# Optimization experiments

Hardware: AMD Instinct MI355X
Metric: run time of the kernel (lower is better)

Reference implementation:

```python
import jax, jax.numpy as jnp
import numpy as np

B, L, D_MODEL = 2, 1024, 512
N_LAYERS = 4
D_INNER = 2 * D_MODEL          # expand=2
D_STATE = 16
D_CONV = 4
DT_RANK = D_MODEL // 16        # ceil(512/16)=32
EPS = 1e-5


def layernorm(x, w, b):
    m = jnp.mean(x, axis=-1, keepdims=True)
    v = jnp.var(x, axis=-1, keepdims=True)
    return (x - m) * jax.lax.rsqrt(v + EPS) * w + b


def selective_scan(u, delta, A, Bm, Cm, Dp):
    # u, delta: [b,l,d]; Bm, Cm: [b,l,n]; A: [d,n]; Dp: [d]
    def step(h, inp):
        dt_t, b_t, c_t, u_t = inp            # [b,d],[b,n],[b,n],[b,d]
        dA = jnp.exp(dt_t[:, :, None] * A)   # [b,d,n]
        h = dA * h + (dt_t * u_t)[:, :, None] * b_t[:, None, :]
        y = jnp.einsum('bdn,bn->bd', h, c_t)
        return h, y

    b, l, d = u.shape
    n = A.shape[1]
    h0 = jnp.zeros((b, d, n), u.dtype)
    xs = (jnp.swapaxes(delta, 0, 1), jnp.swapaxes(Bm, 0, 1),
          jnp.swapaxes(Cm, 0, 1), jnp.swapaxes(u, 0, 1))
    _, ys = jax.lax.scan(step, h0, xs)       # ys: [l,b,d]
    return jnp.swapaxes(ys, 0, 1) + u * Dp


def mamba(x, in_w, conv_w, conv_b, xp_w, dtp_w, dtp_b, A_log, Dp, out_w):
    # x: [b,l,D_MODEL]
    xz = x @ in_w.T                          # [b,l,2*d_inner]
    xc, z = jnp.split(xz, 2, axis=-1)
    xc = jnp.swapaxes(xc, 1, 2)              # [b,d_inner,l]
    xc = jax.lax.conv_general_dilated(
        xc, conv_w[:, None, :], (1,), [(D_CONV - 1, 0)],
        feature_group_count=D_INNER,
        dimension_numbers=('NCH', 'OIH', 'NCH')) + conv_b[None, :, None]
    xc = jax.nn.silu(jnp.swapaxes(xc, 1, 2))  # [b,l,d_inner]
    x_dbl = xc @ xp_w.T                       # [b,l,dt_rank+2n]
    dt = x_dbl[..., :DT_RANK]
    Bm = x_dbl[..., DT_RANK:DT_RANK + D_STATE]
    Cm = x_dbl[..., DT_RANK + D_STATE:]
    dt = jax.nn.softplus(dt @ dtp_w.T + dtp_b)
    A = -jnp.exp(A_log)
    y = selective_scan(xc, dt, A, Bm, Cm, Dp)
    y = y * jax.nn.silu(z)
    return y @ out_w.T


def forward(x, in_proj_w, conv_w, conv_b, x_proj_w, dt_proj_w, dt_proj_b,
            A_log, D_param, out_proj_w, ln_w, ln_b, fnorm_w, fnorm_b):
    residual = None
    for i in range(in_proj_w.shape[0]):
        residual = x if residual is None else x + residual
        xn = layernorm(x, ln_w[i], ln_b[i])  # norm of incoming x (as in torch src)
        h1 = mamba(xn, in_proj_w[i, 0], conv_w[i, 0], conv_b[i, 0],
                   x_proj_w[i, 0], dt_proj_w[i, 0], dt_proj_b[i, 0],
                   A_log[i, 0], D_param[i, 0], out_proj_w[i, 0])
        h2 = mamba(jnp.flip(xn, axis=1), in_proj_w[i, 1], conv_w[i, 1],
                   conv_b[i, 1], x_proj_w[i, 1], dt_proj_w[i, 1],
                   dt_proj_b[i, 1], A_log[i, 1], D_param[i, 1],
                   out_proj_w[i, 1])
        x = h1 + h2                           # bi_add: NOT flipped back, faithful
    x = x + residual
    return layernorm(x, fnorm_w, fnorm_b)


def setup_inputs() -> dict:
    key = jax.random.key(0)
    ks = jax.random.split(key, 8)
    P2 = (N_LAYERS, 2)
    inp = {}
    inp['x'] = jax.random.normal(ks[0], (B, L, D_MODEL), jnp.float32)
    inp['in_proj_w'] = jax.random.normal(ks[1], P2 + (2 * D_INNER, D_MODEL), jnp.float32) * 0.02
    inp['conv_w'] = jax.random.normal(ks[2], P2 + (D_INNER, D_CONV), jnp.float32) * 0.1
    inp['conv_b'] = jnp.zeros(P2 + (D_INNER,), jnp.float32)
    inp['x_proj_w'] = jax.random.normal(ks[3], P2 + (DT_RANK + 2 * D_STATE, D_INNER), jnp.float32) * 0.02
    inp['dt_proj_w'] = jax.random.normal(ks[4], P2 + (D_INNER, DT_RANK), jnp.float32) * (DT_RANK ** -0.5)
    inp['dt_proj_b'] = jnp.full(P2 + (D_INNER,), float(np.log(np.expm1(0.01))), jnp.float32)
    inp['A_log'] = jnp.broadcast_to(jnp.log(jnp.arange(1, D_STATE + 1, dtype=jnp.float32)), P2 + (D_INNER, D_STATE)).copy()
    inp['D_param'] = jnp.ones(P2 + (D_INNER,), jnp.float32)
    inp['out_proj_w'] = jax.random.normal(ks[5], P2 + (D_MODEL, D_INNER), jnp.float32) * 0.02
    inp['ln_w'] = jnp.ones((N_LAYERS, D_MODEL), jnp.float32)
    inp['ln_b'] = jnp.zeros((N_LAYERS, D_MODEL), jnp.float32)
    inp['fnorm_w'] = jnp.ones((D_MODEL,), jnp.float32)
    inp['fnorm_b'] = jnp.zeros((D_MODEL,), jnp.float32)
    return inp


def reference(x, in_proj_w, conv_w, conv_b, x_proj_w, dt_proj_w, dt_proj_b,
              A_log, D_param, out_proj_w, ln_w, ln_b, fnorm_w, fnorm_b):
    return forward(x, in_proj_w, conv_w, conv_b, x_proj_w, dt_proj_w,
                   dt_proj_b, A_log, D_param, out_proj_w, ln_w, ln_b,
                   fnorm_w, fnorm_b)
```

## Files before the change

kernel.cpp:

```cpp
#include <hip/hip_runtime.h>
#include <hip/hip_bf16.h>
#include <type_traits>

#define B_   2
#define L_   1024
#define DM   512
#define DI   1024
#define DS   16
#define DTR  32
#define ROWS (B_*L_)
#define NCH  16
#define CHUNK (L_/NCH)

#define PO_CW    0
#define PO_CB    32768
#define PO_XPW   40960
#define PO_DTW   565248
#define PO_DTB   827392
#define PO_ALOG  835584
#define PO_DP    966656
#define PO_LNW   974848
#define PO_LNB   976896
#define PO_FNW   978944
#define PO_FNB   979456
#define PO_END   979968

#define N_WIN    (4*2097152)
#define N_WOUT   (4*1048576)
#define N_X      1048576

typedef __bf16 bf16x8 __attribute__((ext_vector_type(8)));
typedef float  f32x4  __attribute__((ext_vector_type(4)));
using bf16 = __hip_bfloat16;

__device__ __forceinline__ bf16x8 ld8(const bf16* p){
    return *reinterpret_cast<const bf16x8*>(p);
}
__device__ __forceinline__ float b2f(bf16 v){ return __bfloat162float(v); }

__device__ __forceinline__ unsigned pkbf2(float a, float b){
    bf16 ha = __float2bfloat16(a), hb = __float2bfloat16(b);
    unsigned short ua = *(unsigned short*)&ha, ub = *(unsigned short*)&hb;
    return (unsigned)ua | ((unsigned)ub << 16);
}
__device__ __forceinline__ float unpk_lo(unsigned v){
    unsigned x = v << 16; return __builtin_bit_cast(float, x);
}
__device__ __forceinline__ float unpk_hi(unsigned v){
    unsigned x = v & 0xffff0000u; return __builtin_bit_cast(float, x);
}

__device__ __forceinline__ void async_cp16(const bf16* g, bf16* s){
    __builtin_amdgcn_global_load_lds(
        (const __attribute__((address_space(1))) unsigned int*)g,
        (__attribute__((address_space(3))) unsigned int*)s, 16, 0, 0);
}

__global__ void detect_kernel(const void* Dp_raw, int* flag){
    *flag = (*(const unsigned int*)Dp_raw == 0x3F800000u) ? 1 : 0;
}

__device__ __forceinline__ bf16 cvload(const void* s, long o, int f){
    return f ? __float2bfloat16(((const float*)s)[o]) : ((const bf16*)s)[o];
}

__global__ void megacvt_kernel(const void* cw, const void* cb, const void* xpw,
                               const void* dtw, const void* dtb, const void* al,
                               const void* dp, const void* lnw, const void* lnb,
                               const void* fnw, const void* fnb,
                               const void* inw, const void* outw, const void* xin,
                               bf16* PP, bf16* WIN, bf16* WOUT,
                               float* X, float* R, const int* flag){
    long i = (long)blockIdx.x*256 + threadIdx.x;
    int f = *flag;
    if (i < PO_END){
        const void* s; long o;
        if      (i < PO_CB)   { s = cw;  o = i; }
        else if (i < PO_XPW)  { s = cb;  o = i - PO_CB; }
        else if (i < PO_DTW)  { s = xpw; o = i - PO_XPW; }
        else if (i < PO_DTB)  { s = dtw; o = i - PO_DTW; }
        else if (i < PO_ALOG) { s = dtb; o = i - PO_DTB; }
        else if (i < PO_DP)   { s = al;  o = i - PO_ALOG; }
        else if (i < PO_LNW)  { s = dp;  o = i - PO_DP; }
        else if (i < PO_LNB)  { s = lnw; o = i - PO_LNW; }
        else if (i < PO_FNW)  { s = lnb; o = i - PO_LNB; }
        else if (i < PO_FNB)  { s = fnw; o = i - PO_FNW; }
        else                  { s = fnb; o = i - PO_FNB; }
        PP[i] = cvload(s, o, f);
        return;
    }
    i -= PO_END;
    if (i < N_WIN){ WIN[i] = cvload(inw, i, f); return; }
    i -= N_WIN;
    if (i < N_WOUT){
        long l = i >> 20, r = i & 1048575;
        long n = r >> 11, dir = (r >> 10) & 1, d = r & 1023;
        WOUT[i] = cvload(outw, ((l*2 + dir)*512 + n)*1024 + d, f);
        return;
    }
    i -= N_WOUT;
    if (i < N_X){
        X[i] = f ? ((const float*)xin)[i] : b2f(((const bf16*)xin)[i]);
        R[i] = 0.f;
    }
}

__global__ void ln_kernel(const float* __restrict__ P, int nparts,
                          float* __restrict__ R,
                          const bf16* __restrict__ w, const bf16* __restrict__ b,
                          void* __restrict__ out, int mode, const int* flag){
    int row = blockIdx.x, lane = threadIdx.x;
    size_t base = (size_t)row*DM + lane*8;
    float v[8];
    *(float4*)&v[0] = *(const float4*)(P+base);
    *(float4*)&v[4] = *(const float4*)(P+base+4);
    for (int k=1; k<nparts; ++k){
        float4 a0 = *(const float4*)(P + (size_t)k*1048576 + base);
        float4 a1 = *(const float4*)(P + (size_t)k*1048576 + base + 4);
        v[0]+=a0.x; v[1]+=a0.y; v[2]+=a0.z; v[3]+=a0.w;
        v[4]+=a1.x; v[5]+=a1.y; v[6]+=a1.z; v[7]+=a1.w;
    }
    if (mode == 0){
        float4 r0 = *(const float4*)(R+base);
        float4 r1 = *(const float4*)(R+base+4);
        r0.x += v[0]; r0.y += v[1]; r0.z += v[2]; r0.w += v[3];
        r1.x += v[4]; r1.y += v[5]; r1.z += v[6]; r1.w += v[7];
        *(float4*)(R+base)   = r0;
        *(float4*)(R+base+4) = r1;
    } else {
        float4 r0 = *(const float4*)(R+base);
        float4 r1 = *(const float4*)(R+base+4);
        v[0]+=r0.x; v[1]+=r0.y; v[2]+=r0.z; v[3]+=r0.w;
        v[4]+=r1.x; v[5]+=r1.y; v[6]+=r1.z; v[7]+=r1.w;
    }
    float s=0.f, sq=0.f;
    #pragma unroll
    for (int j=0;j<8;++j){ s += v[j]; sq += v[j]*v[j]; }
    #pragma unroll
    for (int off=32; off>=1; off>>=1){
        s  += __shfl_xor(s,  off, 64);
        sq += __shfl_xor(sq, off, 64);
    }
    float mean = s*(1.f/DM);
    float var  = sq*(1.f/DM) - mean*mean;
    float rs   = rsqrtf(var + 1e-5f);
    bf16x8 wv = ld8(w + lane*8), bv = ld8(b + lane*8);
    float res[8];
    #pragma unroll
    for (int j=0;j<8;++j)
        res[j] = (v[j]-mean)*rs*(float)wv[j] + (float)bv[j];
    if (mode == 1 && *flag){
        float* of = (float*)out;
        *(float4*)(of+base)   = make_float4(res[0],res[1],res[2],res[3]);
        *(float4*)(of+base+4) = make_float4(res[4],res[5],res[6],res[7]);
    } else {
        union { bf16 h[8]; uint4 u; } o;
        #pragma unroll
        for (int j=0;j<8;++j) o.h[j] = __float2bfloat16(res[j]);
        *(uint4*)((bf16*)out + base) = o.u;
    }
}

template<int WM, int WN, int SK, typename CT>
__global__ __launch_bounds__(WM*WN*64)
void gemm_lds(const bf16* __restrict__ A, const bf16* __restrict__ W,
              CT* __restrict__ C, int K, int lda, int ldw, int ldc,
              int selTiles, long wSel){
    constexpr int BM = WM*64, BN = WN*64, T = WM*WN*64;
    constexpr int RA = (BM*4)/T, RB = (BN*4)/T;
    __shared__ __align__(16) bf16 sA[BM*32];
    __shared__ __align__(16) bf16 sB[BN*32];
    int tid = threadIdx.x;
    int mtile = blockIdx.y, ntile = blockIdx.x;
    if (mtile >= selTiles) W += wSel;
    int m0 = mtile*BM, n0 = ntile*BN;
    int kPer = K/SK, kBeg = blockIdx.z*kPer, kEnd = kBeg + kPer;
    if (SK > 1)
        C += (size_t)blockIdx.z * (size_t)(gridDim.y*BM) * (size_t)(gridDim.x*BN);
    int wave = tid>>6, lane = tid&63, quad = lane>>4, r = lane&15;
    int wrow = wave / WN, wcol = wave % WN;
    const bf16* Abase = A + (size_t)m0*lda;
    const bf16* Wbase = W + (size_t)n0*ldw;
    f32x4 acc[4][4] = {};
    for (int k0 = kBeg; k0 < kEnd; k0 += 32){
        #pragma unroll
        for (int rr=0; rr<RA; ++rr){
            int q = rr*T + tid;
            async_cp16(Abase + (size_t)(q>>2)*lda + k0 + (q&3)*8, &sA[q*8]);
        }
        #pragma unroll
        for (int rr=0; rr<RB; ++rr){
            int q = rr*T + tid;
            async_cp16(Wbase + (size_t)(q>>2)*ldw + k0 + (q&3)*8, &sB[q*8]);
        }
        __syncthreads();
        bf16x8 af[4], bw[4];
        #pragma unroll
        for (int mt=0; mt<4; ++mt)
            af[mt] = *(const bf16x8*)&sA[(wrow*64 + mt*16 + r)*32 + quad*8];
        #pragma unroll
        for (int nt=0; nt<4; ++nt)
            bw[nt] = *(const bf16x8*)&sB[(wcol*64 + nt*16 + r)*32 + quad*8];
        #pragma unroll
        for (int mt=0; mt<4; ++mt)
            #pragma unroll
            for (int nt=0; nt<4; ++nt)
                acc[mt][nt] = __builtin_amdgcn_mfma_f32_16x16x32_bf16(
                    af[mt], bw[nt], acc[mt][nt], 0,0,0);
        __syncthreads();
    }
    #pragma unroll
    for (int mt=0; mt<4; ++mt){
        #pragma unroll
        for (int nt=0; nt<4; ++nt){
            int col = n0 + wcol*64 + nt*16 + r;
            #pragma unroll
            for (int ri=0; ri<4; ++ri){
                int row = m0 + wrow*64 + mt*16 + quad*4 + ri;
                size_t idx = (size_t)row*ldc + col;
                if constexpr (std::is_same<CT, bf16>::value)
                    C[idx] = __float2bfloat16(acc[mt][nt][ri]);
                else
                    C[idx] = acc[mt][nt][ri];
            }
        }
    }
}

__global__ void reduce_xd(const float* __restrict__ P, float* __restrict__ XD){
    int i = blockIdx.x*256 + threadIdx.x;
    float s = 0.f;
    #pragma unroll
    for (int k=0;k<8;++k) s += P[k*262144 + i];
    int j = i & 63, grow = i >> 6, dir = grow >> 11, row = grow & 2047;
    XD[row*128 + dir*64 + j] = s;
}

__global__ void conv_kernel(const bf16* __restrict__ XZ, const bf16* __restrict__ cw,
                            const bf16* __restrict__ cb, bf16* __restrict__ XC){
    int id  = blockIdx.x*256 + threadIdx.x;
    int d   = id & (DI-1);
    int t   = (id >> 10) & (L_-1);
    int b   = (id >> 20) & 1;
    int dir = id >> 21;
    float wv[4];
    #pragma unroll
    for (int k=0;k<4;++k) wv[k] = b2f(cw[((size_t)dir*DI + d)*4 + k]);
    float acc = b2f(cb[dir*DI + d]);
    #pragma unroll
    for (int k=0;k<4;++k){
        int tau = t - 3 + k;
        if (tau >= 0){
            int sig = dir ? (L_-1-tau) : tau;
            acc += wv[k] * b2f(XZ[((size_t)(b*L_ + sig))*4096 + dir*2048 + d]);
        }
    }
    float s = acc * (1.f/(1.f + __expf(-acc)));
    XC[((size_t)dir*ROWS + (size_t)b*L_ + t)*DI + d] = __float2bfloat16(s);
}

__global__ void dtproj_kernel(const float* __restrict__ XD, const bf16* __restrict__ dtw,
                              const bf16* __restrict__ dtb, bf16* __restrict__ DT){
    int id  = blockIdx.x*256 + threadIdx.x;
    int d   = id & (DI-1);
    int row = (id >> 10) & (ROWS-1);
    int dir = id >> 21;
    const float* xr = XD + (size_t)row*128 + dir*64;
    const bf16*  wp = dtw + ((size_t)dir*DI + d)*DTR;
    float acc = b2f(dtb[dir*DI + d]);
    #pragma unroll
    for (int kk=0;kk<4;++kk){
        bf16x8 wv = ld8(wp + kk*8);
        #pragma unroll
        for (int j=0;j<8;++j) acc += xr[kk*8+j]*(float)wv[j];
    }
    float sp = acc > 20.f ? acc : log1pf(__expf(acc));
    DT[((size_t)dir*ROWS + row)*DI + d] = __float2bfloat16(sp);
}

template<int PHASE>
__global__ __launch_bounds__(256)
void scan_phase(const bf16* __restrict__ DT, const bf16* __restrict__ XC,
                const float* __restrict__ XD, const bf16* __restrict__ XZ,
                const bf16* __restrict__ Al, const bf16* __restrict__ Dp,
                float* __restrict__ SP, float* __restrict__ SH,
                bf16* __restrict__ Y){
    int dirb = blockIdx.z, dir = dirb >> 1, b = dirb & 1;
    int c    = blockIdx.y;
    int d0   = blockIdx.x*128;
    int tid  = threadIdx.x;
    int dl   = tid >> 1, nh = tid & 1;
    int d    = d0 + dl;

    __shared__ unsigned sDTW[CHUNK][128];
    __shared__ float sBC[CHUNK][32];
    __shared__ unsigned sGU[(PHASE==3) ? CHUNK*128 : 1];

    #pragma unroll
    for (int it=0; it<2; ++it){
        int idx = it*256 + tid;
        int t = idx >> 3, j = idx & 7;
        const float* src = XD + ((size_t)(b*L_) + c*CHUNK + t)*128 + dir*64 + 32 + j*4;
        *(float4*)&sBC[t][j*4] = *(const float4*)src;
    }
    {
        int dcol = tid & 127;
        float Dval = (PHASE==3) ? b2f(Dp[dir*DI + d0 + dcol]) : 0.f;
        #pragma unroll 8
        for (int it=0; it<32; ++it){
            int idx = it*256 + tid;
            int t = idx >> 7;
            int tg = c*CHUNK + t;
            size_t row = (size_t)b*L_ + tg;
            size_t gidx = ((size_t)dir*ROWS + row)*DI + d0 + dcol;
            float dt = b2f(DT[gidx]);
            float u  = b2f(XC[gidx]);
            sDTW[t][dcol] = pkbf2(dt, dt*u);
            if (PHASE == 3){
                size_t zrow = dir ? ((size_t)b*L_ + (L_-1-tg)) : row;
                float zv = b2f(XZ[zrow*4096 + dir*2048 + 1024 + d0 + dcol]);
                float g  = zv*(1.f/(1.f + __expf(-zv)));
                sGU[t*128 + dcol] = pkbf2(g, u*Dval*g);
            }
        }
    }

    float An[8];
    {
        const bf16* ap = Al + ((size_t)dir*DI + d)*DS + nh*8;
        bf16x8 av = ld8(ap);
        #pragma unroll
        for (int j=0;j<8;++j) An[j] = -__expf((float)av[j]);
    }

    float h[8], pr[8];
    size_t so = ((size_t)(dirb*NCH + c)*DI + d)*DS + nh*8;
    #pragma unroll
    for (int j=0;j<8;++j){ h[j]=0.f; pr[j]=1.f; }
    if (PHASE == 3){
        for (int cc=0; cc<c; ++cc){
            size_t o = ((size_t)(dirb*NCH + cc)*DI + d)*DS + nh*8;
            f32x4 p0 = *(const f32x4*)&SP[o];
            f32x4 p1 = *(const f32x4*)&SP[o+4];
            f32x4 h0 = *(const f32x4*)&SH[o];
            f32x4 h1 = *(const f32x4*)&SH[o+4];
            #pragma unroll
            for (int j=0;j<4;++j){
                h[j]   = p0[j]*h[j]   + h0[j];
                h[4+j] = p1[j]*h[4+j] + h1[j];
            }
        }
    }
    __syncthreads();

    bf16* Yp = Y + ((size_t)b*L_ + c*CHUNK)*2048 + dir*DI + d;

    for (int tl=0; tl<CHUNK; ++tl){
        unsigned dw = sDTW[tl][dl];
        float dtv = unpk_lo(dw), wv = unpk_hi(dw);
        const float* Bp = &sBC[tl][nh*8];
        float y = 0.f;
        #pragma unroll
        for (int j=0;j<8;++j){
            float dA = __expf(dtv*An[j]);
            h[j] = dA*h[j] + wv*Bp[j];
            if (PHASE == 1) pr[j] *= dA;
            else            y += h[j]*Bp[16+j];
        }
        if (PHASE == 3){
            y += __shfl_xor(y, 1, 64);
            if (nh == 0){
                unsigned gu = sGU[tl*128 + dl];
                Yp[(size_t)tl*2048] = __float2bfloat16(y*unpk_lo(gu) + unpk_hi(gu));
            }
        }
    }
    if (PHASE == 1){
        *(f32x4*)&SP[so]   = *(f32x4*)&pr[0];
        *(f32x4*)&SP[so+4] = *(f32x4*)&pr[4];
        *(f32x4*)&SH[so]   = *(f32x4*)&h[0];
        *(f32x4*)&SH[so+4] = *(f32x4*)&h[4];
    }
}

extern "C" void kernel_launch(void* const* d_in, const int* in_sizes, int n_in,
                              void* d_out, int out_size, void* d_ws, size_t ws_size,
                              hipStream_t stream){
    const void* x_raw    = d_in[0];
    const void* inw_raw  = d_in[1];
    const void* convw_raw= d_in[2];
    const void* convb_raw= d_in[3];
    const void* xpw_raw  = d_in[4];
    const void* dtw_raw  = d_in[5];
    const void* dtb_raw  = d_in[6];
    const void* alog_raw = d_in[7];
    const void* dp_raw   = d_in[8];
    const void* outw_raw = d_in[9];
    const void* lnw_raw  = d_in[10];
    const void* lnb_raw  = d_in[11];
    const void* fnw_raw  = d_in[12];
    const void* fnb_raw  = d_in[13];

    char* ws = (char*)d_ws;
    float* X   = (float*)(ws + 0);
    float* R   = (float*)(ws + 4194304);
    bf16*  XN  = (bf16*) (ws + 8388608);
    bf16*  XZ  = (bf16*) (ws + 10485760);
    bf16*  XC  = (bf16*) (ws + 27262976);
    float* XD  = (float*)(ws + 35651584);
    bf16*  DT  = (bf16*) (ws + 36700160);
    bf16*  Y   = (bf16*) (ws + 44040192);
    float* SP  = (float*)(ws + 52428800);
    float* SH  = (float*)(ws + 56623104);
    bf16*  PP  = (bf16*) (ws + 60817408);
    bf16*  WIN = (bf16*) (ws + 62914560);
    bf16*  WOUT= (bf16*) (ws + 79691776);
    float* PX  = (float*)(ws + 88080384);
    float* PO  = (float*)(ws + 96468992);
    int*   FLAG= (int*)  (ws + 113246208);

    detect_kernel<<<1,1,0,stream>>>(dp_raw, FLAG);
    {
        long total = (long)PO_END + N_WIN + N_WOUT + N_X;
        int blocks = (int)((total + 255)/256);
        megacvt_kernel<<<blocks,256,0,stream>>>(
            convw_raw, convb_raw, xpw_raw, dtw_raw, dtb_raw, alog_raw, dp_raw,
            lnw_raw, lnb_raw, fnw_raw, fnb_raw, inw_raw, outw_raw, x_raw,
            PP, WIN, WOUT, X, R, FLAG);
    }

    for (int l=0; l<4; ++l){
        ln_kernel<<<ROWS,64,0,stream>>>(l==0 ? X : PO, l==0 ? 1 : 4, R,
                                        PP+PO_LNW+l*DM, PP+PO_LNB+l*DM, XN, 0, FLAG);

        gemm_lds<2,2,1,bf16><<<dim3(32,16,1),256,0,stream>>>(
            XN, WIN + (size_t)l*2097152, XZ, 512, 512, 512, 4096, 1<<30, 0);

        conv_kernel<<<16384,256,0,stream>>>(XZ, PP+PO_CW + (size_t)l*2*DI*4,
                                            PP+PO_CB + l*2*DI, XC);

        gemm_lds<2,1,8,float><<<dim3(1,32,8),128,0,stream>>>(
            XC, PP+PO_XPW + (size_t)l*2*64*DI, PX, 1024, 1024, 1024, 64,
            16, (long)64*DI);
        reduce_xd<<<1024,256,0,stream>>>(PX, XD);

        dtproj_kernel<<<16384,256,0,stream>>>(XD, PP+PO_DTW + (size_t)l*2*DI*DTR,
                                              PP+PO_DTB + l*2*DI, DT);

        scan_phase<1><<<dim3(DI/128,NCH,4),256,0,stream>>>(
            DT, XC, XD, XZ, PP+PO_ALOG + (size_t)l*2*DI*DS, PP+PO_DP + l*2*DI,
            SP, SH, Y);
        scan_phase<3><<<dim3(DI/128,NCH,4),256,0,stream>>>(
            DT, XC, XD, XZ, PP+PO_ALOG + (size_t)l*2*DI*DS, PP+PO_DP + l*2*DI,
            SP, SH, Y);

        gemm_lds<2,2,4,float><<<dim3(4,16,4),256,0,stream>>>(
            Y, WOUT + (size_t)l*1048576, PO, 2048, 2048, 2048, 512, 1<<30, 0);
    }

    ln_kernel<<<ROWS,64,0,stream>>>(PO, 4, R, PP+PO_FNW, PP+PO_FNB, d_out, 1, FLAG);
}
```

Baseline: 742.7 us.

## Pack dt and dt*u in dtproj, halve scan LDS, compute chunk decay from dt sum

dtproj now writes a packed bf16 pair (dt, dt*u) so the scan kernels load one word instead of separate DT and XC values. The scan processes each chunk in two halves of 32 steps, which shrinks shared memory, and sets launch bounds to 4 blocks per SM for higher occupancy. Phase 1 no longer multiplies out the decay product at every step; it sums dt and takes one exp at the end. Phase 3 stages partial outputs in LDS and applies the z gating and D skip term in a separate coalesced epilogue. The cost is a larger DTW buffer, an extra XC read in dtproj, and more syncthreads per chunk.

```diff
diff --git a/kernel.cpp b/kernel.cpp
--- a/kernel.cpp
+++ b/kernel.cpp
@@ -11,6 +11,7 @@
 #define ROWS (B_*L_)
 #define NCH  16
 #define CHUNK (L_/NCH)
+#define HC   32
 
 #define PO_CW    0
 #define PO_CB    32768
@@ -260,7 +261,8 @@
 }
 
 __global__ void dtproj_kernel(const float* __restrict__ XD, const bf16* __restrict__ dtw,
-                              const bf16* __restrict__ dtb, bf16* __restrict__ DT){
+                              const bf16* __restrict__ dtb, const bf16* __restrict__ XC,
+                              unsigned* __restrict__ DTW){
     int id  = blockIdx.x*256 + threadIdx.x;
     int d   = id & (DI-1);
     int row = (id >> 10) & (ROWS-1);
@@ -275,12 +277,14 @@
         for (int j=0;j<8;++j) acc += xr[kk*8+j]*(float)wv[j];
     }
     float sp = acc > 20.f ? acc : log1pf(__expf(acc));
-    DT[((size_t)dir*ROWS + row)*DI + d] = __float2bfloat16(sp);
+    size_t idx = ((size_t)dir*ROWS + row)*DI + d;
+    float u = b2f(XC[idx]);
+    DTW[idx] = pkbf2(sp, sp*u);
 }
 
 template<int PHASE>
-__global__ __launch_bounds__(256)
-void scan_phase(const bf16* __restrict__ DT, const bf16* __restrict__ XC,
+__global__ __launch_bounds__(256,4)
+void scan_phase(const unsigned* __restrict__ DTW, const bf16* __restrict__ XC,
                 const float* __restrict__ XD, const bf16* __restrict__ XZ,
                 const bf16* __restrict__ Al, const bf16* __restrict__ Dp,
                 float* __restrict__ SP, float* __restrict__ SH,
@@ -291,39 +295,11 @@
     int tid  = threadIdx.x;
     int dl   = tid >> 1, nh = tid & 1;
     int d    = d0 + dl;
-
-    __shared__ unsigned sDTW[CHUNK][128];
-    __shared__ float sBC[CHUNK][32];
-    __shared__ unsigned sGU[(PHASE==3) ? CHUNK*128 : 1];
-
-    #pragma unroll
-    for (int it=0; it<2; ++it){
-        int idx = it*256 + tid;
-        int t = idx >> 3, j = idx & 7;
-        const float* src = XD + ((size_t)(b*L_) + c*CHUNK + t)*128 + dir*64 + 32 + j*4;
-        *(float4*)&sBC[t][j*4] = *(const float4*)src;
-    }
-    {
-        int dcol = tid & 127;
-        float Dval = (PHASE==3) ? b2f(Dp[dir*DI + d0 + dcol]) : 0.f;
-        #pragma unroll 8
-        for (int it=0; it<32; ++it){
-            int idx = it*256 + tid;
-            int t = idx >> 7;
-            int tg = c*CHUNK + t;
-            size_t row = (size_t)b*L_ + tg;
-            size_t gidx = ((size_t)dir*ROWS + row)*DI + d0 + dcol;
-            float dt = b2f(DT[gidx]);
-            float u  = b2f(XC[gidx]);
-            sDTW[t][dcol] = pkbf2(dt, dt*u);
-            if (PHASE == 3){
-                size_t zrow = dir ? ((size_t)b*L_ + (L_-1-tg)) : row;
-                float zv = b2f(XZ[zrow*4096 + dir*2048 + 1024 + d0 + dcol]);
-                float g  = zv*(1.f/(1.f + __expf(-zv)));
-                sGU[t*128 + dcol] = pkbf2(g, u*Dval*g);
-            }
-        }
-    }
+    int dcol = tid & 127;
+
+    __shared__ unsigned sDTW[HC][128];
+    __shared__ float    sBC[HC][32];
+    __shared__ bf16     sOutH[(PHASE==3) ? 2*HC*128 : 2];
 
     float An[8];
     {
@@ -333,10 +309,10 @@
         for (int j=0;j<8;++j) An[j] = -__expf((float)av[j]);
     }
 
-    float h[8], pr[8];
+    float h[8], S = 0.f;
+    #pragma unroll
+    for (int j=0;j<8;++j) h[j] = 0.f;
     size_t so = ((size_t)(dirb*NCH + c)*DI + d)*DS + nh*8;
-    #pragma unroll
-    for (int j=0;j<8;++j){ h[j]=0.f; pr[j]=1.f; }
     if (PHASE == 3){
         for (int cc=0; cc<c; ++cc){
             size_t o = ((size_t)(dirb*NCH + cc)*DI + d)*DS + nh*8;
@@ -351,31 +327,68 @@
             }
         }
     }
-    __syncthreads();
-
-    bf16* Yp = Y + ((size_t)b*L_ + c*CHUNK)*2048 + dir*DI + d;
-
-    for (int tl=0; tl<CHUNK; ++tl){
-        unsigned dw = sDTW[tl][dl];
-        float dtv = unpk_lo(dw), wv = unpk_hi(dw);
-        const float* Bp = &sBC[tl][nh*8];
-        float y = 0.f;
-        #pragma unroll
-        for (int j=0;j<8;++j){
-            float dA = __expf(dtv*An[j]);
-            h[j] = dA*h[j] + wv*Bp[j];
-            if (PHASE == 1) pr[j] *= dA;
-            else            y += h[j]*Bp[16+j];
-        }
+
+    const unsigned* DTWb = DTW + ((size_t)dir*ROWS + b*L_ + c*CHUNK)*DI + d0;
+    float Dv = (PHASE==3) ? b2f(Dp[dir*DI + d0 + dcol]) : 0.f;
+
+    for (int hc=0; hc<2; ++hc){
+        {
+            int t0 = tid >> 7;
+            #pragma unroll
+            for (int it=0; it<16; ++it){
+                int t = it*2 + t0;
+                sDTW[t][dcol] = DTWb[(size_t)(hc*HC + t)*DI + dcol];
+            }
+        }
+        #pragma unroll
+        for (int it=0; it<4; ++it){
+            int idx = it*256 + tid;
+            int t = idx >> 5, j = idx & 31;
+            sBC[t][j] = XD[((size_t)(b*L_) + c*CHUNK + hc*HC + t)*128 + dir*64 + 32 + j];
+        }
+        __syncthreads();
+
+        #pragma unroll 4
+        for (int tl=0; tl<HC; ++tl){
+            unsigned dw = sDTW[tl][dl];
+            float dtv = unpk_lo(dw), wv = unpk_hi(dw);
+            const float* Bp = &sBC[tl][nh*8];
+            float y = 0.f;
+            if (PHASE == 1) S += dtv;
+            #pragma unroll
+            for (int j=0;j<8;++j){
+                float dA = __expf(dtv*An[j]);
+                h[j] = dA*h[j] + wv*Bp[j];
+                if (PHASE == 3) y += h[j]*Bp[16+j];
+            }
+            if (PHASE == 3)
+                sOutH[(nh*HC + tl)*128 + dl] = __float2bfloat16(y);
+        }
+
         if (PHASE == 3){
-            y += __shfl_xor(y, 1, 64);
-            if (nh == 0){
-                unsigned gu = sGU[tl*128 + dl];
-                Yp[(size_t)tl*2048] = __float2bfloat16(y*unpk_lo(gu) + unpk_hi(gu));
+            __syncthreads();
+            int t0 = tid >> 7;
+            #pragma unroll
+            for (int it=0; it<16; ++it){
+                int t = it*2 + t0;
+                int tg = c*CHUNK + hc*HC + t;
+                size_t row = (size_t)b*L_ + tg;
+                float y = b2f(sOutH[t*128 + dcol]) + b2f(sOutH[(HC + t)*128 + dcol]);
+                size_t zrow = dir ? ((size_t)b*L_ + (L_-1-tg)) : row;
+                float zv = b2f(XZ[zrow*4096 + dir*2048 + 1024 + d0 + dcol]);
+                float g  = zv*(1.f/(1.f + __expf(-zv)));
+                float u  = b2f(XC[((size_t)dir*ROWS + row)*DI + d0 + dcol]);
+                Y[row*2048 + (size_t)dir*DI + d0 + dcol] =
+                    __float2bfloat16(y*g + u*Dv*g);
             }
         }
-    }
+        __syncthreads();
+    }
+
     if (PHASE == 1){
+        float pr[8];
+        #pragma unroll
+        for (int j=0;j<8;++j) pr[j] = __expf(An[j]*S);
         *(f32x4*)&SP[so]   = *(f32x4*)&pr[0];
         *(f32x4*)&SP[so+4] = *(f32x4*)&pr[4];
         *(f32x4*)&SH[so]   = *(f32x4*)&h[0];
@@ -402,22 +415,22 @@
     const void* fnb_raw  = d_in[13];
 
     char* ws = (char*)d_ws;
-    float* X   = (float*)(ws + 0);
-    float* R   = (float*)(ws + 4194304);
-    bf16*  XN  = (bf16*) (ws + 8388608);
-    bf16*  XZ  = (bf16*) (ws + 10485760);
-    bf16*  XC  = (bf16*) (ws + 27262976);
-    float* XD  = (float*)(ws + 35651584);
-    bf16*  DT  = (bf16*) (ws + 36700160);
-    bf16*  Y   = (bf16*) (ws + 44040192);
-    float* SP  = (float*)(ws + 52428800);
-    float* SH  = (float*)(ws + 56623104);
-    bf16*  PP  = (bf16*) (ws + 60817408);
-    bf16*  WIN = (bf16*) (ws + 62914560);
-    bf16*  WOUT= (bf16*) (ws + 79691776);
-    float* PX  = (float*)(ws + 88080384);
-    float* PO  = (float*)(ws + 96468992);
-    int*   FLAG= (int*)  (ws + 113246208);
+    float*    X   = (float*)   (ws + 0);
+    float*    R   = (float*)   (ws + 4194304);
+    bf16*     XN  = (bf16*)    (ws + 8388608);
+    bf16*     XZ  = (bf16*)    (ws + 10485760);
+    bf16*     XC  = (bf16*)    (ws + 27262976);
+    float*    XD  = (float*)   (ws + 35651584);
+    unsigned* DTW = (unsigned*)(ws + 36700160);
+    bf16*     Y   = (bf16*)    (ws + 53477376);
+    float*    SP  = (float*)   (ws + 61865984);
+    float*    SH  = (float*)   (ws + 66060288);
+    bf16*     PP  = (bf16*)    (ws + 70254592);
+    bf16*     WIN = (bf16*)    (ws + 72351744);
+    bf16*     WOUT= (bf16*)    (ws + 89128960);
+    float*    PX  = (float*)   (ws + 97517568);
+    float*    PO  = (float*)   (ws + 105906176);
+    int*      FLAG= (int*)     (ws + 122683392);
 
     detect_kernel<<<1,1,0,stream>>>(dp_raw, FLAG);
     {
@@ -445,13 +458,13 @@
         reduce_xd<<<1024,256,0,stream>>>(PX, XD);
 
         dtproj_kernel<<<16384,256,0,stream>>>(XD, PP+PO_DTW + (size_t)l*2*DI*DTR,
-                                              PP+PO_DTB + l*2*DI, DT);
+                                              PP+PO_DTB + l*2*DI, XC, DTW);
 
         scan_phase<1><<<dim3(DI/128,NCH,4),256,0,stream>>>(
-            DT, XC, XD, XZ, PP+PO_ALOG + (size_t)l*2*DI*DS, PP+PO_DP + l*2*DI,
+            DTW, XC, XD, XZ, PP+PO_ALOG + (size_t)l*2*DI*DS, PP+PO_DP + l*2*DI,
             SP, SH, Y);
         scan_phase<3><<<dim3(DI/128,NCH,4),256,0,stream>>>(
-            DT, XC, XD, XZ, PP+PO_ALOG + (size_t)l*2*DI*DS, PP+PO_DP + l*2*DI,
+            DTW, XC, XD, XZ, PP+PO_ALOG + (size_t)l*2*DI*DS, PP+PO_DP + l*2*DI,
             SP, SH, Y);
 
         gemm_lds<2,2,4,float><<<dim3(4,16,4),256,0,stream>>>(
```

Measured after the change: 819.9 us. +10.4%, slower.

## Precompute packed dt/dt*u and gate terms upstream, async-load scan chunks, double chunk count

Applied to the files above, without the earlier changes.

The packed (dt, dt*u) pair is now computed in the dt-projection kernel, and the packed (silu(z), u*D*silu(z)) pair in the conv kernel. Both are written to new workspace buffers. The two scan phases then load these precomputed words straight into LDS with global_load_lds async copies, replacing the per-element conversion and gating work done during scan staging. The scan is also split into 32 chunks instead of 16 to raise parallelism. In exchange the intermediate buffers are 32-bit rather than bf16, adding global traffic, and the serial prefix loop over previous chunk states gets longer.

```diff
diff --git a/kernel.cpp b/kernel.cpp
--- a/kernel.cpp
+++ b/kernel.cpp
@@ -9,7 +9,7 @@
 #define DS   16
 #define DTR  32
 #define ROWS (B_*L_)
-#define NCH  16
+#define NCH  32
 #define CHUNK (L_/NCH)
 
 #define PO_CW    0
@@ -50,7 +50,7 @@
     unsigned x = v & 0xffff0000u; return __builtin_bit_cast(float, x);
 }
 
-__device__ __forceinline__ void async_cp16(const bf16* g, bf16* s){
+__device__ __forceinline__ void async_cp16(const void* g, void* s){
     __builtin_amdgcn_global_load_lds(
         (const __attribute__((address_space(1))) unsigned int*)g,
         (__attribute__((address_space(3))) unsigned int*)s, 16, 0, 0);
@@ -237,7 +237,8 @@
 }
 
 __global__ void conv_kernel(const bf16* __restrict__ XZ, const bf16* __restrict__ cw,
-                            const bf16* __restrict__ cb, bf16* __restrict__ XC){
+                            const bf16* __restrict__ cb, const bf16* __restrict__ Dp,
+                            bf16* __restrict__ XC, unsigned* __restrict__ GU){
     int id  = blockIdx.x*256 + threadIdx.x;
     int d   = id & (DI-1);
     int t   = (id >> 10) & (L_-1);
@@ -255,12 +256,19 @@
             acc += wv[k] * b2f(XZ[((size_t)(b*L_ + sig))*4096 + dir*2048 + d]);
         }
     }
-    float s = acc * (1.f/(1.f + __expf(-acc)));
-    XC[((size_t)dir*ROWS + (size_t)b*L_ + t)*DI + d] = __float2bfloat16(s);
+    float u = acc * (1.f/(1.f + __expf(-acc)));
+    size_t idx = ((size_t)dir*ROWS + (size_t)b*L_ + t)*DI + d;
+    XC[idx] = __float2bfloat16(u);
+    int sig3 = dir ? (L_-1-t) : t;
+    float zv = b2f(XZ[((size_t)(b*L_ + sig3))*4096 + dir*2048 + 1024 + d]);
+    float g  = zv*(1.f/(1.f + __expf(-zv)));
+    float Dv = b2f(Dp[dir*DI + d]);
+    GU[idx] = pkbf2(g, u*Dv*g);
 }
 
 __global__ void dtproj_kernel(const float* __restrict__ XD, const bf16* __restrict__ dtw,
-                              const bf16* __restrict__ dtb, bf16* __restrict__ DT){
+                              const bf16* __restrict__ dtb, const bf16* __restrict__ XC,
+                              unsigned* __restrict__ DTW){
     int id  = blockIdx.x*256 + threadIdx.x;
     int d   = id & (DI-1);
     int row = (id >> 10) & (ROWS-1);
@@ -275,14 +283,15 @@
         for (int j=0;j<8;++j) acc += xr[kk*8+j]*(float)wv[j];
     }
     float sp = acc > 20.f ? acc : log1pf(__expf(acc));
-    DT[((size_t)dir*ROWS + row)*DI + d] = __float2bfloat16(sp);
+    size_t idx = ((size_t)dir*ROWS + row)*DI + d;
+    float u = b2f(XC[idx]);
+    DTW[idx] = pkbf2(sp, sp*u);
 }
 
 template<int PHASE>
 __global__ __launch_bounds__(256)
-void scan_phase(const bf16* __restrict__ DT, const bf16* __restrict__ XC,
-                const float* __restrict__ XD, const bf16* __restrict__ XZ,
-                const bf16* __restrict__ Al, const bf16* __restrict__ Dp,
+void scan_phase(const unsigned* __restrict__ DTW, const unsigned* __restrict__ GU,
+                const float* __restrict__ XD, const bf16* __restrict__ Al,
                 float* __restrict__ SP, float* __restrict__ SH,
                 bf16* __restrict__ Y){
     int dirb = blockIdx.z, dir = dirb >> 1, b = dirb & 1;
@@ -292,37 +301,30 @@
     int dl   = tid >> 1, nh = tid & 1;
     int d    = d0 + dl;
 
-    __shared__ unsigned sDTW[CHUNK][128];
-    __shared__ float sBC[CHUNK][32];
-    __shared__ unsigned sGU[(PHASE==3) ? CHUNK*128 : 1];
-
-    #pragma unroll
-    for (int it=0; it<2; ++it){
-        int idx = it*256 + tid;
-        int t = idx >> 3, j = idx & 7;
-        const float* src = XD + ((size_t)(b*L_) + c*CHUNK + t)*128 + dir*64 + 32 + j*4;
-        *(float4*)&sBC[t][j*4] = *(const float4*)src;
+    __shared__ __align__(16) unsigned sDTW[CHUNK*128];
+    __shared__ __align__(16) float    sBC[CHUNK][32];
+    __shared__ __align__(16) unsigned sGU[(PHASE==3)?CHUNK*128:4];
+
+    const unsigned* DTWb = DTW + ((size_t)dir*ROWS + b*L_ + c*CHUNK)*DI + d0;
+    #pragma unroll
+    for (int it=0; it<4; ++it){
+        int q = it*256 + tid;
+        int t = q >> 5, c4 = q & 31;
+        async_cp16(DTWb + (size_t)t*DI + c4*4, &sDTW[q*4]);
+    }
+    if (PHASE == 3){
+        const unsigned* GUb = GU + ((size_t)dir*ROWS + b*L_ + c*CHUNK)*DI + d0;
+        #pragma unroll
+        for (int it=0; it<4; ++it){
+            int q = it*256 + tid;
+            int t = q >> 5, c4 = q & 31;
+            async_cp16(GUb + (size_t)t*DI + c4*4, &sGU[q*4]);
+        }
     }
     {
-        int dcol = tid & 127;
-        float Dval = (PHASE==3) ? b2f(Dp[dir*DI + d0 + dcol]) : 0.f;
-        #pragma unroll 8
-        for (int it=0; it<32; ++it){
-            int idx = it*256 + tid;
-            int t = idx >> 7;
-            int tg = c*CHUNK + t;
-            size_t row = (size_t)b*L_ + tg;
-            size_t gidx = ((size_t)dir*ROWS + row)*DI + d0 + dcol;
-            float dt = b2f(DT[gidx]);
-            float u  = b2f(XC[gidx]);
-            sDTW[t][dcol] = pkbf2(dt, dt*u);
-            if (PHASE == 3){
-                size_t zrow = dir ? ((size_t)b*L_ + (L_-1-tg)) : row;
-                float zv = b2f(XZ[zrow*4096 + dir*2048 + 1024 + d0 + dcol]);
-                float g  = zv*(1.f/(1.f + __expf(-zv)));
-                sGU[t*128 + dcol] = pkbf2(g, u*Dval*g);
-            }
-        }
+        int t = tid >> 3, j = tid & 7;
+        async_cp16(XD + ((size_t)(b*L_) + c*CHUNK + t)*128 + dir*64 + 32 + j*4,
+                   &sBC[t][j*4]);
     }
 
     float An[8];
@@ -334,9 +336,9 @@
     }
 
     float h[8], pr[8];
+    #pragma unroll
+    for (int j=0;j<8;++j){ h[j]=0.f; pr[j]=1.f; }
     size_t so = ((size_t)(dirb*NCH + c)*DI + d)*DS + nh*8;
-    #pragma unroll
-    for (int j=0;j<8;++j){ h[j]=0.f; pr[j]=1.f; }
     if (PHASE == 3){
         for (int cc=0; cc<c; ++cc){
             size_t o = ((size_t)(dirb*NCH + cc)*DI + d)*DS + nh*8;
@@ -355,8 +357,9 @@
 
     bf16* Yp = Y + ((size_t)b*L_ + c*CHUNK)*2048 + dir*DI + d;
 
+    #pragma unroll 4
     for (int tl=0; tl<CHUNK; ++tl){
-        unsigned dw = sDTW[tl][dl];
+        unsigned dw = sDTW[tl*128 + dl];
         float dtv = unpk_lo(dw), wv = unpk_hi(dw);
         const float* Bp = &sBC[tl][nh*8];
         float y = 0.f;
@@ -402,22 +405,23 @@
     const void* fnb_raw  = d_in[13];
 
     char* ws = (char*)d_ws;
-    float* X   = (float*)(ws + 0);
-    float* R   = (float*)(ws + 4194304);
-    bf16*  XN  = (bf16*) (ws + 8388608);
-    bf16*  XZ  = (bf16*) (ws + 10485760);
-    bf16*  XC  = (bf16*) (ws + 27262976);
-    float* XD  = (float*)(ws + 35651584);
-    bf16*  DT  = (bf16*) (ws + 36700160);
-    bf16*  Y   = (bf16*) (ws + 44040192);
-    float* SP  = (float*)(ws + 52428800);
-    float* SH  = (float*)(ws + 56623104);
-    bf16*  PP  = (bf16*) (ws + 60817408);
-    bf16*  WIN = (bf16*) (ws + 62914560);
-    bf16*  WOUT= (bf16*) (ws + 79691776);
-    float* PX  = (float*)(ws + 88080384);
-    float* PO  = (float*)(ws + 96468992);
-    int*   FLAG= (int*)  (ws + 113246208);
+    float*    X   = (float*)   (ws + 0);
+    float*    R   = (float*)   (ws + 4194304);
+    bf16*     XN  = (bf16*)    (ws + 8388608);
+    bf16*     XZ  = (bf16*)    (ws + 10485760);
+    bf16*     XC  = (bf16*)    (ws + 27262976);
+    float*    XD  = (float*)   (ws + 35651584);
+    unsigned* DTW = (unsigned*)(ws + 36700160);
+    unsigned* GU  = (unsigned*)(ws + 52428800);
+    bf16*     Y   = (bf16*)    (ws + 68157440);
+    float*    SP  = (float*)   (ws + 76546048);
+    float*    SH  = (float*)   (ws + 84934656);
+    bf16*     PP  = (bf16*)    (ws + 93323264);
+    bf16*     WIN = (bf16*)    (ws + 95420416);
+    bf16*     WOUT= (bf16*)    (ws + 112197632);
+    float*    PX  = (float*)   (ws + 120586240);
+    float*    PO  = (float*)   (ws + 128974848);
+    int*      FLAG= (int*)     (ws + 145752064);
 
     detect_kernel<<<1,1,0,stream>>>(dp_raw, FLAG);
     {
@@ -437,7 +441,8 @@
             XN, WIN + (size_t)l*2097152, XZ, 512, 512, 512, 4096, 1<<30, 0);
 
         conv_kernel<<<16384,256,0,stream>>>(XZ, PP+PO_CW + (size_t)l*2*DI*4,
-                                            PP+PO_CB + l*2*DI, XC);
+                                            PP+PO_CB + l*2*DI, PP+PO_DP + l*2*DI,
+                                            XC, GU);
 
         gemm_lds<2,1,8,float><<<dim3(1,32,8),128,0,stream>>>(
             XC, PP+PO_XPW + (size_t)l*2*64*DI, PX, 1024, 1024, 1024, 64,
@@ -445,14 +450,12 @@
         reduce_xd<<<1024,256,0,stream>>>(PX, XD);
 
         dtproj_kernel<<<16384,256,0,stream>>>(XD, PP+PO_DTW + (size_t)l*2*DI*DTR,
-                                              PP+PO_DTB + l*2*DI, DT);
+                                              PP+PO_DTB + l*2*DI, XC, DTW);
 
         scan_phase<1><<<dim3(DI/128,NCH,4),256,0,stream>>>(
-            DT, XC, XD, XZ, PP+PO_ALOG + (size_t)l*2*DI*DS, PP+PO_DP + l*2*DI,
-            SP, SH, Y);
+            DTW, GU, XD, PP+PO_ALOG + (size_t)l*2*DI*DS, SP, SH, Y);
         scan_phase<3><<<dim3(DI/128,NCH,4),256,0,stream>>>(
-            DT, XC, XD, XZ, PP+PO_ALOG + (size_t)l*2*DI*DS, PP+PO_DP + l*2*DI,
-            SP, SH, Y);
+            DTW, GU, XD, PP+PO_ALOG + (size_t)l*2*DI*DS, SP, SH, Y);
 
         gemm_lds<2,2,4,float><<<dim3(4,16,4),256,0,stream>>>(
             Y, WOUT + (size_t)l*1048576, PO, 2048, 2048, 2048, 512, 1<<30, 0);
```

Measured after the change: 771.2 us. 1.04x slower.
